# Optimization experiments

Measured on AMD Instinct MI355X. Metric: run time of the kernel, lower is better.

Reference implementation:

```python
import jax, jax.numpy as jnp
import numpy as np

DIM = 2048
DT_RANK = 32
D_STATE = 16
DEPTH = 12


def setup_inputs() -> dict:
    key = jax.random.key(0)
    ks = jax.random.split(key, 8)
    d, r, n, L = DIM, DT_RANK, D_STATE, DEPTH
    s = 0.02
    return {
        "x": jax.random.normal(ks[0], (1, 3, d), jnp.float32),
        "norm_g": jnp.ones((L, d), jnp.float32),
        "norm_b": jnp.zeros((L, d), jnp.float32),
        "proj_w": jax.random.normal(ks[1], (L, d, d), jnp.float32) * s,
        "proj_b": jnp.zeros((L, d), jnp.float32),
        "fconv_w": jax.random.normal(ks[2], (L, d, d), jnp.float32) * s,  # Conv1d k=1 == dxd matmul
        "fconv_b": jnp.zeros((L, d), jnp.float32),
        "bconv_w": jax.random.normal(ks[3], (L, d, d), jnp.float32) * s,
        "bconv_b": jnp.zeros((L, d), jnp.float32),
        "dbc_w": jax.random.normal(ks[4], (L, r + 2 * n, d), jnp.float32) * s,  # x_proj (no bias)
        "dtp_w": jax.random.normal(ks[5], (L, d, r), jnp.float32) * s,          # dt_proj weight
        "dtp_b": jnp.zeros((L, d), jnp.float32),
        "A_log": jnp.broadcast_to(jnp.log(jnp.arange(1, n + 1, dtype=jnp.float32)), (L, d, n)) + jnp.zeros((L, d, n), jnp.float32),
        "Dp": jnp.ones((L, d), jnp.float32),
    }


def _ln(x, g, b):
    mu = x.mean(-1, keepdims=True)
    var = ((x - mu) ** 2).mean(-1, keepdims=True)
    return (x - mu) * jax.lax.rsqrt(var + 1e-5) * g + b


def _ssm(u, dbc_w, dtp_w, dtp_b, A_log, Dp):
    # selective scan: u (b,s,d); A_log (d,n); dbc_w (r+2n,d); dtp_w (d,r)
    r, n = DT_RANK, D_STATE
    A = -jnp.exp(A_log)                                    # (d,n)
    dbc = jnp.einsum('bsd,ed->bse', u, dbc_w)              # (b,s,r+2n)
    delta = jax.nn.softplus(jnp.einsum('bsr,dr->bsd', dbc[..., :r], dtp_w) + dtp_b)  # (b,s,d)
    B = dbc[..., r:r + n]                                  # (b,s,n)
    C = dbc[..., r + n:]                                   # (b,s,n)
    dA = jnp.exp(jnp.einsum('bsd,dn->bsdn', delta, A))     # (b,s,d,n)
    dBu = jnp.einsum('bsd,bsn,bsd->bsdn', delta, B, u)     # (b,s,d,n)

    def step(h, t):
        dA_t, dBu_t, C_t = t
        h = dA_t * h + dBu_t                               # (b,d,n)
        return h, jnp.einsum('bdn,bn->bd', h, C_t)

    h0 = jnp.zeros((u.shape[0], u.shape[2], n), u.dtype)
    _, ys = jax.lax.scan(step, h0, (jnp.swapaxes(dA, 0, 1), jnp.swapaxes(dBu, 0, 1), jnp.swapaxes(C, 0, 1)))
    return jnp.swapaxes(ys, 0, 1) + u * Dp                 # (b,s,d)


def _block(x, p):
    skip = x
    xn = _ln(x, p['norm_g'], p['norm_b'])
    z1 = jnp.einsum('bsd,ed->bse', xn, p['proj_w']) + p['proj_b']   # proj; note x1 == z1 (same layer applied twice)
    f = jnp.einsum('bsd,ed->bse', z1, p['fconv_w']) + p['fconv_b']  # forward conv1d (k=1)
    bw = jnp.einsum('bsd,ed->bse', z1, p['bconv_w']) + p['bconv_b'] # backward conv1d (k=1)
    y1 = _ssm(f, p['dbc_w'], p['dtp_w'], p['dtp_b'], p['A_log'], p['Dp'])
    y2 = _ssm(bw, p['dbc_w'], p['dtp_w'], p['dtp_b'], p['A_log'], p['Dp'])
    z = jax.nn.silu(z1)
    return (y1 + y2) * z + skip


_PNAMES = ['norm_g', 'norm_b', 'proj_w', 'proj_b', 'fconv_w', 'fconv_b', 'bconv_w', 'bconv_b', 'dbc_w', 'dtp_w', 'dtp_b', 'A_log', 'Dp']


def reference(x, norm_g, norm_b, proj_w, proj_b, fconv_w, fconv_b, bconv_w, bconv_b, dbc_w, dtp_w, dtp_b, A_log, Dp):
    # three streams x[0][0..2], each (1,1,d); batch as b=3, s=1 (per-token ops => equivalent)
    xb = x[0, :3][:, None, :]  # (3,1,d)
    vals = [norm_g, norm_b, proj_w, proj_b, fconv_w, fconv_b, bconv_w, bconv_b, dbc_w, dtp_w, dtp_b, A_log, Dp]
    out = xb
    for i in range(DEPTH):
        p = {k: v[i] for k, v in zip(_PNAMES, vals)}
        out = _block(xb, p)  # faithful: original feeds the SAME input to every layer; only last layer's output survives
    return jnp.swapaxes(out, 0, 1)  # (1,3,d) == cat((a,b,c), dim=1)
```

## Files before the change

### kernel.cpp

```cpp
#include <hip/hip_runtime.h>
#include <math.h>

constexpr int D     = 2048;
constexpr int LAYER = 11;
constexpr int BATCH = 3;

__global__ __launch_bounds__(256) void k_ln_proj(const float* __restrict__ x,
                                                 const float* __restrict__ g,
                                                 const float* __restrict__ bt,
                                                 const float* __restrict__ W,
                                                 const float* __restrict__ bias,
                                                 float* __restrict__ z1) {
    const int tid  = threadIdx.x;
    const int wave = tid >> 6;
    const int lane = tid & 63;

    __shared__ float xn_s[BATCH * D];
    __shared__ float wred[6][4];

    float s0 = 0.f, s1 = 0.f, s2 = 0.f, q0 = 0.f, q1 = 0.f, q2 = 0.f;
    for (int i = tid; i < D; i += 256) {
        float v0 = x[0 * D + i], v1 = x[1 * D + i], v2 = x[2 * D + i];
        s0 += v0; q0 += v0 * v0;
        s1 += v1; q1 += v1 * v1;
        s2 += v2; q2 += v2 * v2;
    }
#pragma unroll
    for (int off = 32; off; off >>= 1) {
        s0 += __shfl_down(s0, off); q0 += __shfl_down(q0, off);
        s1 += __shfl_down(s1, off); q1 += __shfl_down(q1, off);
        s2 += __shfl_down(s2, off); q2 += __shfl_down(q2, off);
    }
    if (lane == 0) {
        wred[0][wave] = s0; wred[1][wave] = q0;
        wred[2][wave] = s1; wred[3][wave] = q1;
        wred[4][wave] = s2; wred[5][wave] = q2;
    }
    __syncthreads();
    const float S0 = wred[0][0] + wred[0][1] + wred[0][2] + wred[0][3];
    const float Q0 = wred[1][0] + wred[1][1] + wred[1][2] + wred[1][3];
    const float S1 = wred[2][0] + wred[2][1] + wred[2][2] + wred[2][3];
    const float Q1 = wred[3][0] + wred[3][1] + wred[3][2] + wred[3][3];
    const float S2 = wred[4][0] + wred[4][1] + wred[4][2] + wred[4][3];
    const float Q2 = wred[5][0] + wred[5][1] + wred[5][2] + wred[5][3];
    const float inv = 1.f / D;
    const float mu0 = S0 * inv, mu1 = S1 * inv, mu2 = S2 * inv;
    const float r0 = rsqrtf(Q0 * inv - mu0 * mu0 + 1e-5f);
    const float r1 = rsqrtf(Q1 * inv - mu1 * mu1 + 1e-5f);
    const float r2 = rsqrtf(Q2 * inv - mu2 * mu2 + 1e-5f);

    for (int i = tid; i < D; i += 256) {
        const float gi = g[i], bi = bt[i];
        xn_s[0 * D + i] = (x[0 * D + i] - mu0) * r0 * gi + bi;
        xn_s[1 * D + i] = (x[1 * D + i] - mu1) * r1 * gi + bi;
        xn_s[2 * D + i] = (x[2 * D + i] - mu2) * r2 * gi + bi;
    }
    __syncthreads();

    const int row = blockIdx.x * 4 + wave;
    const float4* __restrict__ Wr  = (const float4*)(W + (size_t)row * D);
    const float4* __restrict__ in4 = (const float4*)xn_s;

    float a0 = 0.f, a1 = 0.f, a2 = 0.f;
#pragma unroll
    for (int k = 0; k < 8; ++k) {
        const int idx = k * 64 + lane;
        const float4 w  = Wr[idx];
        const float4 x0 = in4[idx];
        const float4 x1 = in4[512 + idx];
        const float4 x2 = in4[1024 + idx];
        a0 += w.x * x0.x + w.y * x0.y + w.z * x0.z + w.w * x0.w;
        a1 += w.x * x1.x + w.y * x1.y + w.z * x1.z + w.w * x1.w;
        a2 += w.x * x2.x + w.y * x2.y + w.z * x2.z + w.w * x2.w;
    }
#pragma unroll
    for (int off = 32; off; off >>= 1) {
        a0 += __shfl_down(a0, off);
        a1 += __shfl_down(a1, off);
        a2 += __shfl_down(a2, off);
    }
    if (lane == 0) {
        const float bs = bias[row];
        z1[0 * D + row] = a0 + bs;
        z1[1 * D + row] = a1 + bs;
        z1[2 * D + row] = a2 + bs;
    }
}

__global__ __launch_bounds__(256) void k_gemv2(const float* __restrict__ in,
                                               const float* __restrict__ W0,
                                               const float* __restrict__ b0,
                                               float* __restrict__ o0,
                                               const float* __restrict__ W1,
                                               const float* __restrict__ b1,
                                               float* __restrict__ o1) {
    const int wave = threadIdx.x >> 6;
    const int lane = threadIdx.x & 63;
    const int m      = blockIdx.x >> 9;
    const int rowblk = blockIdx.x & 511;
    const int row    = rowblk * 4 + wave;

    const float* __restrict__ W    = (m == 0) ? W0 : W1;
    const float* __restrict__ bias = (m == 0) ? b0 : b1;
    float* __restrict__ out        = (m == 0) ? o0 : o1;

    const float4* __restrict__ Wr  = (const float4*)(W + (size_t)row * D);
    const float4* __restrict__ in4 = (const float4*)in;

    float a0 = 0.f, a1 = 0.f, a2 = 0.f;
#pragma unroll
    for (int k = 0; k < 8; ++k) {
        const int idx = k * 64 + lane;
        const float4 w  = Wr[idx];
        const float4 x0 = in4[idx];
        const float4 x1 = in4[512 + idx];
        const float4 x2 = in4[1024 + idx];
        a0 += w.x * x0.x + w.y * x0.y + w.z * x0.z + w.w * x0.w;
        a1 += w.x * x1.x + w.y * x1.y + w.z * x1.z + w.w * x1.w;
        a2 += w.x * x2.x + w.y * x2.y + w.z * x2.z + w.w * x2.w;
    }
#pragma unroll
    for (int off = 32; off; off >>= 1) {
        a0 += __shfl_down(a0, off);
        a1 += __shfl_down(a1, off);
        a2 += __shfl_down(a2, off);
    }
    if (lane == 0) {
        const float bs = bias[row];
        out[0 * D + row] = a0 + bs;
        out[1 * D + row] = a1 + bs;
        out[2 * D + row] = a2 + bs;
    }
}

__device__ __forceinline__ float softplus_f(float v) {
    return fmaxf(v, 0.f) + log1pf(expf(-fabsf(v)));
}

__global__ __launch_bounds__(256) void k_dbc_final(const float* __restrict__ x,
                                                   const float* __restrict__ z1,
                                                   const float* __restrict__ f,
                                                   const float* __restrict__ bw,
                                                   const float* __restrict__ dbcW,
                                                   const float* __restrict__ dtpW,
                                                   const float* __restrict__ dtpB,
                                                   const float* __restrict__ Dp,
                                                   float* __restrict__ out) {
    const int tid = threadIdx.x;
    const int blk = blockIdx.x;
    const int b   = blk >> 3;
    const int e   = ((blk & 7) << 8) + tid;

    __shared__ float dbc_s[2][64];

    {
        const int row  = tid >> 2;
        const int dir  = (tid >> 1) & 1;
        const int half = tid & 1;
        const float* __restrict__ u = dir ? bw : f;
        const float4* __restrict__ Wr = (const float4*)(dbcW + (size_t)row * D + half * (D / 2));
        const float4* __restrict__ u4 = (const float4*)(u + (size_t)b * D + half * (D / 2));

        float4 acc = make_float4(0.f, 0.f, 0.f, 0.f);
#pragma unroll 8
        for (int k = 0; k < 256; ++k) {
            const float4 w = Wr[k];
            const float4 v = u4[k];
            acc.x += w.x * v.x;
            acc.y += w.y * v.y;
            acc.z += w.z * v.z;
            acc.w += w.w * v.w;
        }
        float a = (acc.x + acc.y) + (acc.z + acc.w);
        a += __shfl_xor(a, 1);
        if (half == 0) dbc_s[dir][row] = a;
    }
    __syncthreads();

    float bcf = 0.f, bcb = 0.f;
#pragma unroll
    for (int n = 0; n < 16; ++n) {
        bcf += dbc_s[0][32 + n] * dbc_s[0][48 + n];
        bcb += dbc_s[1][32 + n] * dbc_s[1][48 + n];
    }

    float df = dtpB[e], db = dtpB[e];
    const float* __restrict__ wr = dtpW + (size_t)e * 32;
#pragma unroll
    for (int r = 0; r < 32; ++r) {
        const float w = wr[r];
        df += dbc_s[0][r] * w;
        db += dbc_s[1][r] * w;
    }
    df = softplus_f(df);
    db = softplus_f(db);

    const float fe  = f[b * D + e];
    const float be  = bw[b * D + e];
    const float dpe = Dp[e];
    const float y   = fe * (df * bcf + dpe) + be * (db * bcb + dpe);

    const float z   = z1[b * D + e];
    const float sil = z / (1.f + expf(-z));

    out[b * D + e] = y * sil + x[b * D + e];
}

extern "C" void kernel_launch(void* const* d_in, const int* in_sizes, int n_in,
                              void* d_out, int out_size, void* d_ws, size_t ws_size,
                              hipStream_t stream) {
    const float* x       = (const float*)d_in[0];
    const float* norm_g  = (const float*)d_in[1]  + (size_t)LAYER * D;
    const float* norm_b  = (const float*)d_in[2]  + (size_t)LAYER * D;
    const float* proj_w  = (const float*)d_in[3]  + (size_t)LAYER * D * D;
    const float* proj_b  = (const float*)d_in[4]  + (size_t)LAYER * D;
    const float* fconv_w = (const float*)d_in[5]  + (size_t)LAYER * D * D;
    const float* fconv_b = (const float*)d_in[6]  + (size_t)LAYER * D;
    const float* bconv_w = (const float*)d_in[7]  + (size_t)LAYER * D * D;
    const float* bconv_b = (const float*)d_in[8]  + (size_t)LAYER * D;
    const float* dbc_w   = (const float*)d_in[9]  + (size_t)LAYER * 64 * D;
    const float* dtp_w   = (const float*)d_in[10] + (size_t)LAYER * D * 32;
    const float* dtp_b   = (const float*)d_in[11] + (size_t)LAYER * D;
    const float* Dp      = (const float*)d_in[13] + (size_t)LAYER * D;

    float* out = (float*)d_out;

    float* ws  = (float*)d_ws;
    float* z1  = ws;
    float* fv  = ws + 6144;
    float* bwv = ws + 12288;

    k_ln_proj<<<512, 256, 0, stream>>>(x, norm_g, norm_b, proj_w, proj_b, z1);
    k_gemv2<<<1024, 256, 0, stream>>>(z1, fconv_w, fconv_b, fv,
                                      bconv_w, bconv_b, bwv);
    k_dbc_final<<<24, 256, 0, stream>>>(x, z1, fv, bwv, dbc_w,
                                        dtp_w, dtp_b, Dp, out);
}
```

Measured before the change: 466.3 us.

## Fuse three kernels into one cooperative kernel with grid-wide syncs

Replaces the three launches (LN+proj GEMV, dual conv GEMV, dbc/final) with a single cooperative kernel of 1024 blocks that uses grid.sync between the stages, falling back to the original launches if the cooperative launch fails. The aim is to remove launch overhead and the gaps between kernels. In exchange it pays for grid barriers, and most blocks sit idle in the first and last stages. The 1024-block grid must fit co-resident, and the 24KB of shared memory per block limits occupancy.

```diff
diff --git a/kernel.cpp b/kernel.cpp
--- a/kernel.cpp
+++ b/kernel.cpp
@@ -1,9 +1,210 @@
 #include <hip/hip_runtime.h>
+#include <hip/hip_cooperative_groups.h>
 #include <math.h>
+
+namespace cg = cooperative_groups;
 
 constexpr int D     = 2048;
 constexpr int LAYER = 11;
 constexpr int BATCH = 3;
+
+__device__ __forceinline__ float softplus_f(float v) {
+    return fmaxf(v, 0.f) + log1pf(expf(-fabsf(v)));
+}
+
+__global__ __launch_bounds__(256, 4) void k_fused(
+    const float* __restrict__ x,    const float* __restrict__ g,
+    const float* __restrict__ bt,
+    const float* __restrict__ projW, const float* __restrict__ projB,
+    const float* __restrict__ fW,    const float* __restrict__ fB,
+    const float* __restrict__ bW,    const float* __restrict__ bB,
+    const float* __restrict__ dbcW,  const float* __restrict__ dtpW,
+    const float* __restrict__ dtpB,  const float* __restrict__ Dp,
+    float* __restrict__ z1, float* __restrict__ fv, float* __restrict__ bwv,
+    float* __restrict__ out)
+{
+    cg::grid_group grid = cg::this_grid();
+    const int tid  = threadIdx.x;
+    const int wave = tid >> 6;
+    const int lane = tid & 63;
+
+    __shared__ float xn_s[BATCH * D];
+    __shared__ float wred[6][4];
+
+    if (blockIdx.x < 512) {
+        float s0 = 0.f, s1 = 0.f, s2 = 0.f, q0 = 0.f, q1 = 0.f, q2 = 0.f;
+        for (int i = tid; i < D; i += 256) {
+            float v0 = x[0 * D + i], v1 = x[1 * D + i], v2 = x[2 * D + i];
+            s0 += v0; q0 += v0 * v0;
+            s1 += v1; q1 += v1 * v1;
+            s2 += v2; q2 += v2 * v2;
+        }
+#pragma unroll
+        for (int off = 32; off; off >>= 1) {
+            s0 += __shfl_down(s0, off); q0 += __shfl_down(q0, off);
+            s1 += __shfl_down(s1, off); q1 += __shfl_down(q1, off);
+            s2 += __shfl_down(s2, off); q2 += __shfl_down(q2, off);
+        }
+        if (lane == 0) {
+            wred[0][wave] = s0; wred[1][wave] = q0;
+            wred[2][wave] = s1; wred[3][wave] = q1;
+            wred[4][wave] = s2; wred[5][wave] = q2;
+        }
+        __syncthreads();
+        const float S0 = wred[0][0] + wred[0][1] + wred[0][2] + wred[0][3];
+        const float Q0 = wred[1][0] + wred[1][1] + wred[1][2] + wred[1][3];
+        const float S1 = wred[2][0] + wred[2][1] + wred[2][2] + wred[2][3];
+        const float Q1 = wred[3][0] + wred[3][1] + wred[3][2] + wred[3][3];
+        const float S2 = wred[4][0] + wred[4][1] + wred[4][2] + wred[4][3];
+        const float Q2 = wred[5][0] + wred[5][1] + wred[5][2] + wred[5][3];
+        const float inv = 1.f / D;
+        const float mu0 = S0 * inv, mu1 = S1 * inv, mu2 = S2 * inv;
+        const float r0 = rsqrtf(Q0 * inv - mu0 * mu0 + 1e-5f);
+        const float r1 = rsqrtf(Q1 * inv - mu1 * mu1 + 1e-5f);
+        const float r2 = rsqrtf(Q2 * inv - mu2 * mu2 + 1e-5f);
+
+        for (int i = tid; i < D; i += 256) {
+            const float gi = g[i], bi = bt[i];
+            xn_s[0 * D + i] = (x[0 * D + i] - mu0) * r0 * gi + bi;
+            xn_s[1 * D + i] = (x[1 * D + i] - mu1) * r1 * gi + bi;
+            xn_s[2 * D + i] = (x[2 * D + i] - mu2) * r2 * gi + bi;
+        }
+        __syncthreads();
+
+        const int row = blockIdx.x * 4 + wave;
+        const float4* __restrict__ Wr  = (const float4*)(projW + (size_t)row * D);
+        const float4* __restrict__ in4 = (const float4*)xn_s;
+
+        float a0 = 0.f, a1 = 0.f, a2 = 0.f;
+#pragma unroll
+        for (int k = 0; k < 8; ++k) {
+            const int idx = k * 64 + lane;
+            const float4 w  = Wr[idx];
+            const float4 x0 = in4[idx];
+            const float4 x1 = in4[512 + idx];
+            const float4 x2 = in4[1024 + idx];
+            a0 += w.x * x0.x + w.y * x0.y + w.z * x0.z + w.w * x0.w;
+            a1 += w.x * x1.x + w.y * x1.y + w.z * x1.z + w.w * x1.w;
+            a2 += w.x * x2.x + w.y * x2.y + w.z * x2.z + w.w * x2.w;
+        }
+#pragma unroll
+        for (int off = 32; off; off >>= 1) {
+            a0 += __shfl_down(a0, off);
+            a1 += __shfl_down(a1, off);
+            a2 += __shfl_down(a2, off);
+        }
+        if (lane == 0) {
+            const float bs = projB[row];
+            z1[0 * D + row] = a0 + bs;
+            z1[1 * D + row] = a1 + bs;
+            z1[2 * D + row] = a2 + bs;
+        }
+    }
+
+    __threadfence();
+    grid.sync();
+
+    {
+        const int m      = blockIdx.x >> 9;
+        const int rowblk = blockIdx.x & 511;
+        const int row    = rowblk * 4 + wave;
+
+        const float* __restrict__ W    = m ? bW : fW;
+        const float* __restrict__ bias = m ? bB : fB;
+        float* __restrict__ o          = m ? bwv : fv;
+
+        const float4* __restrict__ Wr  = (const float4*)(W + (size_t)row * D);
+        const float4* __restrict__ in4 = (const float4*)z1;
+
+        float a0 = 0.f, a1 = 0.f, a2 = 0.f;
+#pragma unroll
+        for (int k = 0; k < 8; ++k) {
+            const int idx = k * 64 + lane;
+            const float4 w  = Wr[idx];
+            const float4 x0 = in4[idx];
+            const float4 x1 = in4[512 + idx];
+            const float4 x2 = in4[1024 + idx];
+            a0 += w.x * x0.x + w.y * x0.y + w.z * x0.z + w.w * x0.w;
+            a1 += w.x * x1.x + w.y * x1.y + w.z * x1.z + w.w * x1.w;
+            a2 += w.x * x2.x + w.y * x2.y + w.z * x2.z + w.w * x2.w;
+        }
+#pragma unroll
+        for (int off = 32; off; off >>= 1) {
+            a0 += __shfl_down(a0, off);
+            a1 += __shfl_down(a1, off);
+            a2 += __shfl_down(a2, off);
+        }
+        if (lane == 0) {
+            const float bs = bias[row];
+            o[0 * D + row] = a0 + bs;
+            o[1 * D + row] = a1 + bs;
+            o[2 * D + row] = a2 + bs;
+        }
+    }
+
+    __threadfence();
+    grid.sync();
+
+    if (blockIdx.x < 24) {
+        const int b = blockIdx.x >> 3;
+        const int e = ((blockIdx.x & 7) << 8) + tid;
+
+        float* dbc0 = xn_s;
+        float* dbc1 = xn_s + 64;
+
+        {
+            const int row  = tid >> 2;
+            const int dir  = (tid >> 1) & 1;
+            const int half = tid & 1;
+            const float* __restrict__ u = dir ? bwv : fv;
+            const float4* __restrict__ Wr = (const float4*)(dbcW + (size_t)row * D + half * (D / 2));
+            const float4* __restrict__ u4 = (const float4*)(u + (size_t)b * D + half * (D / 2));
+
+            float4 acc = make_float4(0.f, 0.f, 0.f, 0.f);
+#pragma unroll 8
+            for (int k = 0; k < 256; ++k) {
+                const float4 w = Wr[k];
+                const float4 v = u4[k];
+                acc.x += w.x * v.x;
+                acc.y += w.y * v.y;
+                acc.z += w.z * v.z;
+                acc.w += w.w * v.w;
+            }
+            float a = (acc.x + acc.y) + (acc.z + acc.w);
+            a += __shfl_xor(a, 1);
+            if (half == 0) (dir ? dbc1 : dbc0)[row] = a;
+        }
+        __syncthreads();
+
+        float bcf = 0.f, bcb = 0.f;
+#pragma unroll
+        for (int n = 0; n < 16; ++n) {
+            bcf += dbc0[32 + n] * dbc0[48 + n];
+            bcb += dbc1[32 + n] * dbc1[48 + n];
+        }
+
+        float df = dtpB[e], db = dtpB[e];
+        const float* __restrict__ wr = dtpW + (size_t)e * 32;
+#pragma unroll
+        for (int r = 0; r < 32; ++r) {
+            const float w = wr[r];
+            df += dbc0[r] * w;
+            db += dbc1[r] * w;
+        }
+        df = softplus_f(df);
+        db = softplus_f(db);
+
+        const float fe  = fv[b * D + e];
+        const float be  = bwv[b * D + e];
+        const float dpe = Dp[e];
+        const float y   = fe * (df * bcf + dpe) + be * (db * bcb + dpe);
+
+        const float z   = z1[b * D + e];
+        const float sil = z / (1.f + expf(-z));
+
+        out[b * D + e] = y * sil + x[b * D + e];
+    }
+}
 
 __global__ __launch_bounds__(256) void k_ln_proj(const float* __restrict__ x,
                                                  const float* __restrict__ g,
@@ -131,10 +332,6 @@
         out[1 * D + row] = a1 + bs;
         out[2 * D + row] = a2 + bs;
     }
-}
-
-__device__ __forceinline__ float softplus_f(float v) {
-    return fmaxf(v, 0.f) + log1pf(expf(-fabsf(v)));
 }
 
 __global__ __launch_bounds__(256) void k_dbc_final(const float* __restrict__ x,
@@ -230,9 +427,22 @@
     float* fv  = ws + 6144;
     float* bwv = ws + 12288;
 
-    k_ln_proj<<<512, 256, 0, stream>>>(x, norm_g, norm_b, proj_w, proj_b, z1);
-    k_gemv2<<<1024, 256, 0, stream>>>(z1, fconv_w, fconv_b, fv,
-                                      bconv_w, bconv_b, bwv);
-    k_dbc_final<<<24, 256, 0, stream>>>(x, z1, fv, bwv, dbc_w,
-                                        dtp_w, dtp_b, Dp, out);
-}
+    void* args[] = {
+        (void*)&x, (void*)&norm_g, (void*)&norm_b,
+        (void*)&proj_w, (void*)&proj_b,
+        (void*)&fconv_w, (void*)&fconv_b,
+        (void*)&bconv_w, (void*)&bconv_b,
+        (void*)&dbc_w, (void*)&dtp_w, (void*)&dtp_b, (void*)&Dp,
+        (void*)&z1, (void*)&fv, (void*)&bwv, (void*)&out
+    };
+
+    hipError_t err = hipLaunchCooperativeKernel((void*)k_fused, dim3(1024),
+                                                dim3(256), args, 0, stream);
+    if (err != hipSuccess) {
+        k_ln_proj<<<512, 256, 0, stream>>>(x, norm_g, norm_b, proj_w, proj_b, z1);
+        k_gemv2<<<1024, 256, 0, stream>>>(z1, fconv_w, fconv_b, fv,
+                                          bconv_w, bconv_b, bwv);
+        k_dbc_final<<<24, 256, 0, stream>>>(x, z1, fv, bwv, dbc_w,
+                                            dtp_w, dtp_b, Dp, out);
+    }
+}
```

Measured after the change: 890.8 us. +91.1%, slower.
